# Kernel tuning notes

Measured on AMD Instinct MI355X. Metric: run time of the kernel, lower is better.

Reference implementation:

```python
import jax, jax.numpy as jnp
import numpy as np

N, E = 50000, 800000
IN_C, HID_C, OUT_C = 256, 256, 256


def setup_inputs() -> dict:
    key = jax.random.key(0)
    ks = jax.random.split(key, 8)
    x_piece = jax.random.normal(ks[0], (N, IN_C), dtype=jnp.float32)
    edge_index_piece = jax.random.randint(ks[1], (2, E), 0, N, dtype=jnp.int64)
    batch = jnp.zeros((N,), dtype=jnp.int64)
    def glorot(k, fan_in, fan_out):
        s = jnp.sqrt(6.0 / (fan_in + fan_out)).astype(jnp.float32)
        return jax.random.uniform(k, (fan_in, fan_out), jnp.float32, -s, s)
    return {
        "x_piece": x_piece,
        "edge_index_piece": edge_index_piece,
        "batch": batch,
        "W1": glorot(ks[2], IN_C, HID_C), "b1": jnp.zeros((HID_C,), jnp.float32),
        "W2": glorot(ks[3], HID_C, HID_C), "b2": jnp.zeros((HID_C,), jnp.float32),
        "W3": glorot(ks[4], HID_C, OUT_C), "b3": jnp.zeros((OUT_C,), jnp.float32),
    }


def _gcn_prep(edge_index, n_nodes):
    # add self-loops, compute symmetric normalization (PyG GCNConv default)
    src = jnp.concatenate([edge_index[0], jnp.arange(n_nodes, dtype=edge_index.dtype)])
    dst = jnp.concatenate([edge_index[1], jnp.arange(n_nodes, dtype=edge_index.dtype)])
    deg = jax.ops.segment_sum(jnp.ones_like(dst, dtype=jnp.float32), dst, num_segments=n_nodes)
    deg_inv_sqrt = jnp.where(deg > 0, jax.lax.rsqrt(jnp.maximum(deg, 1.0)), 0.0)
    norm = deg_inv_sqrt[src] * deg_inv_sqrt[dst]  # [E+N]
    return src, dst, norm


def _gcn_layer(x, src, dst, norm, W, b, n_nodes):
    h = x @ W                                   # [N, out] dense transform first
    msg = h[src] * norm[:, None]                # gather + scale
    out = jax.ops.segment_sum(msg, dst, num_segments=n_nodes)  # scatter-add
    return out + b


def reference(x_piece, edge_index_piece, batch, W1, b1, W2, b2, W3, b3):
    n_nodes = x_piece.shape[0]
    src, dst, norm = _gcn_prep(edge_index_piece, n_nodes)
    x = _gcn_layer(x_piece, src, dst, norm, W1, b1, n_nodes)
    x = jax.nn.gelu(x)
    x = _gcn_layer(x, src, dst, norm, W2, b2, n_nodes)
    x = jax.nn.gelu(x)
    x = _gcn_layer(x, src, dst, norm, W3, b3, n_nodes)
    return x
```

## Files before the change

### kernel.cpp

```cpp
#include <hip/hip_runtime.h>
#include <cstdint>
#include <cstddef>

#define CH 256

typedef _Float16 f16x8 __attribute__((ext_vector_type(8)));
typedef _Float16 f16x4 __attribute__((ext_vector_type(4)));
typedef float f32x4 __attribute__((ext_vector_type(4)));
typedef short short8 __attribute__((ext_vector_type(8)));

#define GLOB(x) ((const __attribute__((address_space(1))) void*)(x))
#define LDSP(x) ((__attribute__((address_space(3))) void*)(x))


__device__ __forceinline__ int ld_idx(const void* p, long long i, int w64) {
    if (w64) return (int)((const long long*)p)[i];
    return ((const int*)p)[i];
}

__device__ __forceinline__ float gelu_f(float x) {
    float x3 = x * x * x;
    float t = tanhf(0.7978845608028654f * (x + 0.044715f * x3));
    return 0.5f * x * (1.0f + t);
}


__global__ void k_detect(const void* __restrict__ ei, int* __restrict__ flag, int E) {
    int l = threadIdx.x;
    long long k = ((long long)l * (long long)(E - 1)) / 63;
    int w = ((const int*)ei)[2 * k + 1];
    unsigned long long vote = __ballot(w == 0);
    if (l == 0) *flag = (vote == ~0ULL) ? 1 : 0;
}

__global__ void k_deg(const void* __restrict__ ei, const int* __restrict__ flag,
                      int* __restrict__ deg, int E) {
    int e = blockIdx.x * blockDim.x + threadIdx.x;
    if (e >= E) return;
    int w64 = *flag;
    int d = ld_idx(ei, (long long)E + e, w64);
    atomicAdd(&deg[d], 1);
}

__global__ void k_scan_block(const int* __restrict__ deg, int* __restrict__ rowptr,
                             int* __restrict__ partial, int N) {
    __shared__ int s[256];
    int gid = blockIdx.x * 256 + threadIdx.x;
    int v = (gid < N) ? deg[gid] : 0;
    s[threadIdx.x] = v;
    __syncthreads();
    for (int off = 1; off < 256; off <<= 1) {
        int t = (threadIdx.x >= off) ? s[threadIdx.x - off] : 0;
        __syncthreads();
        s[threadIdx.x] += t;
        __syncthreads();
    }
    if (gid < N) rowptr[gid] = s[threadIdx.x] - v;
    if (threadIdx.x == 255) partial[blockIdx.x] = s[255];
}

__global__ void k_scan_partial(int* __restrict__ partial, int nb) {
    __shared__ int s[256];
    int i = threadIdx.x;
    int v = (i < nb) ? partial[i] : 0;
    s[i] = v;
    __syncthreads();
    for (int off = 1; off < 256; off <<= 1) {
        int t = (i >= off) ? s[i - off] : 0;
        __syncthreads();
        s[i] += t;
        __syncthreads();
    }
    if (i < nb) partial[i] = s[i] - v;
}

__global__ void k_add_off(int* __restrict__ rowptr, const int* __restrict__ partial,
                          const int* __restrict__ deg, float* __restrict__ dis,
                          int N, int E) {
    int gid = blockIdx.x * 256 + threadIdx.x;
    if (gid < N) {
        rowptr[gid] += partial[blockIdx.x];
        dis[gid] = 1.0f / sqrtf((float)(deg[gid] + 1));
    }
    if (gid == 0) rowptr[N] = E;
}

__global__ void k_scatter(const void* __restrict__ ei, const int* __restrict__ flag,
                          const int* __restrict__ rowptr, int* __restrict__ cnt,
                          int* __restrict__ ssrc, int E) {
    int e = blockIdx.x * blockDim.x + threadIdx.x;
    if (e >= E) return;
    int w64 = *flag;
    int s = ld_idx(ei, e, w64);
    int d = ld_idx(ei, (long long)E + e, w64);
    int pos = rowptr[d] + atomicAdd(&cnt[d], 1);
    ssrc[pos] = s;
}


__global__ void k_split_w3(const float* __restrict__ W1, const float* __restrict__ W2,
                           const float* __restrict__ W3, _Float16* __restrict__ Wh1,
                           _Float16* __restrict__ Wh2, _Float16* __restrict__ Wh3) {
    const float* W = (blockIdx.y == 0) ? W1 : (blockIdx.y == 1) ? W2 : W3;
    _Float16*   Wh = (blockIdx.y == 0) ? Wh1 : (blockIdx.y == 1) ? Wh2 : Wh3;
    int k = threadIdx.x;
    int c = blockIdx.x;
    Wh[c * CH + k] = (_Float16)W[k * CH + c];
}


__global__ __launch_bounds__(256) void k_quant_x(const float* __restrict__ x,
                                                 uint8_t* __restrict__ Xout,
                                                 float* __restrict__ sout, int N) {
    int node = blockIdx.x * 4 + threadIdx.y;
    if (node >= N) return;
    int lane = threadIdx.x;
    float4 v = ((const float4*)(x + (size_t)node * CH))[lane];
    float mx = fmaxf(fmaxf(fabsf(v.x), fabsf(v.y)), fmaxf(fabsf(v.z), fabsf(v.w)));
    #pragma unroll
    for (int off = 32; off > 0; off >>= 1)
        mx = fmaxf(mx, __shfl_xor(mx, off));
    float inv = (mx > 0.f) ? (32767.0f / mx) : 0.f;
    short4 q;
    q.x = (short)__float2int_rn(v.x * inv);
    q.y = (short)__float2int_rn(v.y * inv);
    q.z = (short)__float2int_rn(v.z * inv);
    q.w = (short)__float2int_rn(v.w * inv);
    *(short4*)(Xout + (size_t)node * 512 + (size_t)lane * 8) = q;
    if (lane == 0) sout[node] = mx * (1.0f / 32767.0f);
}


#define GM 128
#define GN 128
#define GK 32

__global__ __launch_bounds__(256, 2)
void k_gemm16(const uint8_t* __restrict__ X16, const float* __restrict__ sx,
              const _Float16* __restrict__ Bh, const float* __restrict__ dis,
              uint8_t* __restrict__ H16, float* __restrict__ hcomb, int M) {
    __shared__ __align__(16) char smem[65536];
    short*    lA16 = (short*)smem;
    _Float16* lB   = (_Float16*)(smem + 16384);

    const int tid  = threadIdx.x;
    const int lane = tid & 63;
    const int wid  = tid >> 6;
    const int m0   = blockIdx.x * GM;
    const int n0   = blockIdx.y * GN;
    const int wm   = wid >> 1, wn = wid & 1;
    const int r15  = lane & 15, kg = lane >> 4;

    auto stage = [&](int buf, int k0) {
        #pragma unroll
        for (int c = 0; c < 4; c++) {
            int call = wid * 4 + c;
            int cc = call & 7;
            int L = cc * 64 + lane;
            int row = L >> 2, ch = L & 3;
            int sch = ch ^ ((row >> 1) & 3);
            if (call < 8) {
                int gr = m0 + row; gr = (gr < M) ? gr : (M - 1);
                const uint8_t* g = X16 + (size_t)gr * 512 + (size_t)k0 * 2 + (sch << 4);
                __builtin_amdgcn_global_load_lds(GLOB(g), LDSP(&lA16[buf * 4096 + L * 8]), 16, 0, 0);
            } else {
                const _Float16* g = Bh + (size_t)(n0 + row) * CH + k0 + (sch << 3);
                __builtin_amdgcn_global_load_lds(GLOB(g), LDSP(&lB[buf * 4096 + L * 8]), 16, 0, 0);
            }
        }
    };

    f32x4 acc[4][4];
    #pragma unroll
    for (int i = 0; i < 4; i++)
        #pragma unroll
        for (int n = 0; n < 4; n++)
            acc[i][n] = (f32x4){0.f, 0.f, 0.f, 0.f};

    stage(0, 0);
    __syncthreads();

    for (int ks = 0; ks < 8; ks++) {
        int cur = ks & 1;
        if (ks < 7) stage(cur ^ 1, (ks + 1) * GK);

        f16x8 aq[4], bh[4];
        #pragma unroll
        for (int i = 0; i < 4; i++) {
            int R = wm * 64 + i * 16 + r15;
            int p = kg ^ ((R >> 1) & 3);
            short8 q = *(const short8*)&lA16[cur * 4096 + R * 32 + p * 8];
            #pragma unroll
            for (int j = 0; j < 8; j++)
                aq[i][j] = (_Float16)q[j];
        }
        #pragma unroll
        for (int n = 0; n < 4; n++) {
            int C = wn * 64 + n * 16 + r15;
            int p = kg ^ ((C >> 1) & 3);
            bh[n] = *(const f16x8*)&lB[cur * 4096 + C * GK + p * 8];
        }
        #pragma unroll
        for (int i = 0; i < 4; i++)
            #pragma unroll
            for (int n = 0; n < 4; n++)
                acc[i][n] = __builtin_amdgcn_mfma_f32_16x16x32_f16(aq[i], bh[n], acc[i][n], 0, 0, 0);
        __syncthreads();
    }

    float sC[4][4];
    #pragma unroll
    for (int i = 0; i < 4; i++)
        #pragma unroll
        for (int r = 0; r < 4; r++) {
            int gr = m0 + wm * 64 + i * 16 + kg * 4 + r;
            sC[i][r] = sx[(gr < M) ? gr : (M - 1)];
        }
    #pragma unroll
    for (int i = 0; i < 4; i++)
        #pragma unroll
        for (int n = 0; n < 4; n++)
            #pragma unroll
            for (int r = 0; r < 4; r++)
                acc[i][n][r] *= sC[i][r];

    float mx = 0.f;
    #pragma unroll
    for (int i = 0; i < 4; i++)
        #pragma unroll
        for (int n = 0; n < 4; n++)
            #pragma unroll
            for (int r = 0; r < 4; r++)
                mx = fmaxf(mx, fabsf(acc[i][n][r]));
    #pragma unroll
    for (int off = 32; off > 0; off >>= 1)
        mx = fmaxf(mx, __shfl_xor(mx, off));
    if (lane == 0) ((float*)smem)[wid] = mx;
    __syncthreads();
    float tmax = fmaxf(fmaxf(((float*)smem)[0], ((float*)smem)[1]),
                       fmaxf(((float*)smem)[2], ((float*)smem)[3]));
    float scl = tmax * (1.0f / 32767.0f);
    float inv = (tmax > 0.f) ? (32767.0f / tmax) : 0.f;
    __syncthreads();

    float* ep = (float*)smem + wid * 4096;
    #pragma unroll
    for (int i = 0; i < 4; i++)
        #pragma unroll
        for (int n = 0; n < 4; n++)
            #pragma unroll
            for (int r = 0; r < 4; r++)
                ep[(i * 16 + kg * 4 + r) * 64 + n * 16 + r15] = acc[i][n][r];
    __syncthreads();

    int q = lane & 15;
    int rsub = lane >> 4;
    #pragma unroll
    for (int p = 0; p < 16; p++) {
        int lrow = p * 4 + rsub;
        int grow = m0 + wm * 64 + lrow;
        if (grow < M) {
            int q0 = __float2int_rn(ep[lrow * 64 + q * 4 + 0] * inv);
            int q1 = __float2int_rn(ep[lrow * 64 + q * 4 + 1] * inv);
            int q2 = __float2int_rn(ep[lrow * 64 + q * 4 + 2] * inv);
            int q3 = __float2int_rn(ep[lrow * 64 + q * 4 + 3] * inv);
            uint2 d;
            d.x = (q0 & 0xFFFF) | (q1 << 16);
            d.y = (q2 & 0xFFFF) | (q3 << 16);
            int col = n0 + wn * 64 + q * 4;
            *(uint2*)(H16 + (size_t)grow * 512 + (size_t)col * 2) = d;
        }
    }

    if (tid < GM && m0 + tid < M)
        hcomb[(size_t)(m0 + tid) * 2 + (n0 >> 7)] = scl * dis[m0 + tid];
}


template <int MODE>
__global__ __launch_bounds__(256) void k_agg(const uint8_t* __restrict__ H16,
                                             const float* __restrict__ hcomb,
                                             const float* __restrict__ dis,
                                             const int* __restrict__ rowptr,
                                             const int* __restrict__ ssrc,
                                             const float* __restrict__ bias,
                                             float* __restrict__ out,
                                             uint8_t* __restrict__ Xout,
                                             float* __restrict__ sxout, int N) {
    int node = blockIdx.x * 4 + threadIdx.y;
    if (node >= N) return;
    int lane = threadIdx.x;
    int half = lane >> 5;
    float d = dis[node];
    short4 hv = *(const short4*)(H16 + (size_t)node * 512 + (size_t)lane * 8);
    float wself = d * hcomb[(size_t)node * 2 + half];
    float ax = wself * (float)hv.x, ay = wself * (float)hv.y;
    float az = wself * (float)hv.z, aw = wself * (float)hv.w;
    int s = rowptr[node], e = rowptr[node + 1];
    int j = s;
    for (; j + 8 <= e; j += 8) {
        int p[8];
        #pragma unroll
        for (int t = 0; t < 8; t++) p[t] = ssrc[j + t];
        short4 v[8];
        float sc[8];
        #pragma unroll
        for (int t = 0; t < 8; t++) {
            v[t] = *(const short4*)(H16 + (size_t)p[t] * 512 + (size_t)lane * 8);
            sc[t] = hcomb[(size_t)p[t] * 2 + half];
        }
        #pragma unroll
        for (int t = 0; t < 8; t++) {
            float wn = d * sc[t];
            ax += wn * (float)v[t].x; ay += wn * (float)v[t].y;
            az += wn * (float)v[t].z; aw += wn * (float)v[t].w;
        }
    }
    for (; j < e; j++) {
        int p = ssrc[j];
        float wn = d * hcomb[(size_t)p * 2 + half];
        short4 v = *(const short4*)(H16 + (size_t)p * 512 + (size_t)lane * 8);
        ax += wn * (float)v.x; ay += wn * (float)v.y;
        az += wn * (float)v.z; aw += wn * (float)v.w;
    }
    float4 b = ((const float4*)bias)[lane];
    ax += b.x; ay += b.y; az += b.z; aw += b.w;
    if (MODE == 0) {
        ax = gelu_f(ax); ay = gelu_f(ay); az = gelu_f(az); aw = gelu_f(aw);
        float mx = fmaxf(fmaxf(fabsf(ax), fabsf(ay)), fmaxf(fabsf(az), fabsf(aw)));
        #pragma unroll
        for (int off = 32; off > 0; off >>= 1)
            mx = fmaxf(mx, __shfl_xor(mx, off));
        float inv = (mx > 0.f) ? (32767.0f / mx) : 0.f;
        short4 q;
        q.x = (short)__float2int_rn(ax * inv);
        q.y = (short)__float2int_rn(ay * inv);
        q.z = (short)__float2int_rn(az * inv);
        q.w = (short)__float2int_rn(aw * inv);
        *(short4*)(Xout + (size_t)node * 512 + (size_t)lane * 8) = q;
        if (lane == 0) sxout[node] = mx * (1.0f / 32767.0f);
    } else {
        ((float4*)(out + (size_t)node * CH))[lane] = make_float4(ax, ay, az, aw);
    }
}


extern "C" void kernel_launch(void* const* d_in, const int* in_sizes, int n_in,
                              void* d_out, int out_size, void* d_ws, size_t ws_size,
                              hipStream_t stream) {
    const float* x  = (const float*)d_in[0];
    const void*  ei = d_in[1];
    const float* W1 = (const float*)d_in[3]; const float* b1 = (const float*)d_in[4];
    const float* W2 = (const float*)d_in[5]; const float* b2 = (const float*)d_in[6];
    const float* W3 = (const float*)d_in[7]; const float* b3 = (const float*)d_in[8];

    int N = in_sizes[0] / CH;
    int E = in_sizes[1] / 2;
    float* out = (float*)d_out;

    char* ws = (char*)d_ws;
    auto take = [&](size_t bytes) {
        char* p = ws;
        ws += (bytes + 15) & ~(size_t)15;
        return p;
    };
    uint8_t*  H16    = (uint8_t*) take((size_t)N * 512);
    uint8_t*  Xa     = (uint8_t*) take((size_t)N * 512);
    uint8_t*  Xb     = (uint8_t*) take((size_t)N * 512);
    float*    hcomb  = (float*)   take((size_t)N * 2 * sizeof(float));
    float*    sxa    = (float*)   take((size_t)N * sizeof(float));
    float*    sxb    = (float*)   take((size_t)N * sizeof(float));
    int*      deg    = (int*)     take((size_t)N * sizeof(int));
    float*    dis    = (float*)   take((size_t)N * sizeof(float));
    int*      rowptr = (int*)     take((size_t)(N + 1) * sizeof(int));
    int*      cnt    = (int*)     take((size_t)N * sizeof(int));
    int*      part   = (int*)     take(4096);
    int*      flag   = (int*)     take(16);
    int*      ssrc   = (int*)     take((size_t)E * sizeof(int));
    _Float16* Wh1    = (_Float16*)take((size_t)CH * CH * 2);
    _Float16* Wh2    = (_Float16*)take((size_t)CH * CH * 2);
    _Float16* Wh3    = (_Float16*)take((size_t)CH * CH * 2);

    hipMemsetAsync(deg, 0, (size_t)N * sizeof(int), stream);
    hipMemsetAsync(cnt, 0, (size_t)N * sizeof(int), stream);

    int eb = (E + 255) / 256;
    int nb = (N + 255) / 256;

    k_detect<<<1, 64, 0, stream>>>(ei, flag, E);
    k_deg<<<eb, 256, 0, stream>>>(ei, flag, deg, E);
    k_scan_block<<<nb, 256, 0, stream>>>(deg, rowptr, part, N);
    k_scan_partial<<<1, 256, 0, stream>>>(part, nb);
    k_add_off<<<nb, 256, 0, stream>>>(rowptr, part, deg, dis, N, E);
    k_scatter<<<eb, 256, 0, stream>>>(ei, flag, rowptr, cnt, ssrc, E);

    dim3 wgrid(CH, 3);
    k_split_w3<<<wgrid, CH, 0, stream>>>(W1, W2, W3, Wh1, Wh2, Wh3);

    dim3 qgrid((N + 3) / 4);
    dim3 qblock(64, 4);
    k_quant_x<<<qgrid, qblock, 0, stream>>>(x, Xa, sxa, N);

    dim3 ggrid((N + GM - 1) / GM, CH / GN);
    dim3 agrid((N + 3) / 4);
    dim3 ablock(64, 4);

    k_gemm16<<<ggrid, 256, 0, stream>>>(Xa, sxa, Wh1, dis, H16, hcomb, N);
    k_agg<0><<<agrid, ablock, 0, stream>>>(H16, hcomb, dis, rowptr, ssrc, b1, out, Xb, sxb, N);
    k_gemm16<<<ggrid, 256, 0, stream>>>(Xb, sxb, Wh2, dis, H16, hcomb, N);
    k_agg<0><<<agrid, ablock, 0, stream>>>(H16, hcomb, dis, rowptr, ssrc, b2, out, Xa, sxa, N);
    k_gemm16<<<ggrid, 256, 0, stream>>>(Xa, sxa, Wh3, dis, H16, hcomb, N);
    k_agg<1><<<agrid, ablock, 0, stream>>>(H16, hcomb, dis, rowptr, ssrc, b3, out, Xb, sxb, N);
}
```

Before: 385.6 us.

## Fuse graph preprocessing, weight conversion and input quantization into one cooperative kernel

Replaces eight separate launches and two memsets (detect, degree count, block scan, partial scan, offset add, CSR scatter, weight transpose and x quantization) with a single cooperative kernel that uses grid-wide syncs between phases. Independent work such as weight conversion and x quantization now shares the first phase with zeroing. This removes launch gaps and tail effects of the small kernels. In exchange it adds grid.sync barriers, and it relies on a fixed 1024-block grid being co-resident. That grid size may leave the memory-bound phases with less parallelism than the original full-size grids had.

```diff
diff --git a/kernel.cpp b/kernel.cpp
--- a/kernel.cpp
+++ b/kernel.cpp
@@ -1,8 +1,11 @@
 #include <hip/hip_runtime.h>
+#include <hip/hip_cooperative_groups.h>
 #include <cstdint>
 #include <cstddef>
 
 #define CH 256
+
+namespace cg = cooperative_groups;
 
 typedef _Float16 f16x8 __attribute__((ext_vector_type(8)));
 typedef _Float16 f16x4 __attribute__((ext_vector_type(4)));
@@ -25,109 +28,108 @@
 }
 
 
-__global__ void k_detect(const void* __restrict__ ei, int* __restrict__ flag, int E) {
-    int l = threadIdx.x;
-    long long k = ((long long)l * (long long)(E - 1)) / 63;
-    int w = ((const int*)ei)[2 * k + 1];
-    unsigned long long vote = __ballot(w == 0);
-    if (l == 0) *flag = (vote == ~0ULL) ? 1 : 0;
-}
-
-__global__ void k_deg(const void* __restrict__ ei, const int* __restrict__ flag,
-                      int* __restrict__ deg, int E) {
-    int e = blockIdx.x * blockDim.x + threadIdx.x;
-    if (e >= E) return;
+__global__ __launch_bounds__(256)
+void k_prep(const void* __restrict__ ei, const float* __restrict__ x,
+            const float* __restrict__ W1, const float* __restrict__ W2,
+            const float* __restrict__ W3,
+            int* __restrict__ flag, int* __restrict__ deg, int* __restrict__ cnt,
+            int* __restrict__ rowptr, int* __restrict__ partial, float* __restrict__ dis,
+            int* __restrict__ ssrc, uint8_t* __restrict__ Xa, float* __restrict__ sxa,
+            _Float16* __restrict__ Wh1, _Float16* __restrict__ Wh2,
+            _Float16* __restrict__ Wh3, int N, int E) {
+    cg::grid_group grid = cg::this_grid();
+    const int tid   = threadIdx.x;
+    const int gsize = gridDim.x * 256;
+    const int gid0  = blockIdx.x * 256 + tid;
+    __shared__ int s[256];
+
+    if (blockIdx.x == 0 && tid < 64) {
+        long long k = ((long long)tid * (long long)(E - 1)) / 63;
+        int w = ((const int*)ei)[2 * k + 1];
+        unsigned long long vote = __ballot(w == 0);
+        if (tid == 0) *flag = (vote == ~0ULL) ? 1 : 0;
+    }
+    for (int i = gid0; i < N; i += gsize) { deg[i] = 0; cnt[i] = 0; }
+    for (int i = gid0; i < 3 * CH * CH; i += gsize) {
+        int l = i >> 16;
+        int r = i & 65535;
+        const float* W = (l == 0) ? W1 : (l == 1) ? W2 : W3;
+        _Float16*   Wh = (l == 0) ? Wh1 : (l == 1) ? Wh2 : Wh3;
+        Wh[r] = (_Float16)W[(r & 255) * CH + (r >> 8)];
+    }
+    {
+        int wave = gid0 >> 6, lane = tid & 63;
+        int nwaves = gsize >> 6;
+        for (int node = wave; node < N; node += nwaves) {
+            float4 v = ((const float4*)(x + (size_t)node * CH))[lane];
+            float mx = fmaxf(fmaxf(fabsf(v.x), fabsf(v.y)), fmaxf(fabsf(v.z), fabsf(v.w)));
+            #pragma unroll
+            for (int off = 32; off > 0; off >>= 1)
+                mx = fmaxf(mx, __shfl_xor(mx, off));
+            float inv = (mx > 0.f) ? (32767.0f / mx) : 0.f;
+            short4 q;
+            q.x = (short)__float2int_rn(v.x * inv);
+            q.y = (short)__float2int_rn(v.y * inv);
+            q.z = (short)__float2int_rn(v.z * inv);
+            q.w = (short)__float2int_rn(v.w * inv);
+            *(short4*)(Xa + (size_t)node * 512 + (size_t)lane * 8) = q;
+            if (lane == 0) sxa[node] = mx * (1.0f / 32767.0f);
+        }
+    }
+    grid.sync();
+
     int w64 = *flag;
-    int d = ld_idx(ei, (long long)E + e, w64);
-    atomicAdd(&deg[d], 1);
-}
-
-__global__ void k_scan_block(const int* __restrict__ deg, int* __restrict__ rowptr,
-                             int* __restrict__ partial, int N) {
-    __shared__ int s[256];
-    int gid = blockIdx.x * 256 + threadIdx.x;
-    int v = (gid < N) ? deg[gid] : 0;
-    s[threadIdx.x] = v;
-    __syncthreads();
-    for (int off = 1; off < 256; off <<= 1) {
-        int t = (threadIdx.x >= off) ? s[threadIdx.x - off] : 0;
+    for (int e = gid0; e < E; e += gsize) {
+        int d = ld_idx(ei, (long long)E + e, w64);
+        atomicAdd(&deg[d], 1);
+    }
+    grid.sync();
+
+    int nb = (N + 255) / 256;
+    for (int b = blockIdx.x; b < nb; b += gridDim.x) {
+        int g = b * 256 + tid;
+        int v = (g < N) ? deg[g] : 0;
+        s[tid] = v;
         __syncthreads();
-        s[threadIdx.x] += t;
+        for (int off = 1; off < 256; off <<= 1) {
+            int t = (tid >= off) ? s[tid - off] : 0;
+            __syncthreads();
+            s[tid] += t;
+            __syncthreads();
+        }
+        if (g < N) rowptr[g] = s[tid] - v;
+        if (tid == 255) partial[b] = s[255];
         __syncthreads();
     }
-    if (gid < N) rowptr[gid] = s[threadIdx.x] - v;
-    if (threadIdx.x == 255) partial[blockIdx.x] = s[255];
-}
-
-__global__ void k_scan_partial(int* __restrict__ partial, int nb) {
-    __shared__ int s[256];
-    int i = threadIdx.x;
-    int v = (i < nb) ? partial[i] : 0;
-    s[i] = v;
-    __syncthreads();
-    for (int off = 1; off < 256; off <<= 1) {
-        int t = (i >= off) ? s[i - off] : 0;
+    grid.sync();
+
+    if (blockIdx.x == 0) {
+        int v = (tid < nb) ? partial[tid] : 0;
+        s[tid] = v;
         __syncthreads();
-        s[i] += t;
-        __syncthreads();
-    }
-    if (i < nb) partial[i] = s[i] - v;
-}
-
-__global__ void k_add_off(int* __restrict__ rowptr, const int* __restrict__ partial,
-                          const int* __restrict__ deg, float* __restrict__ dis,
-                          int N, int E) {
-    int gid = blockIdx.x * 256 + threadIdx.x;
-    if (gid < N) {
-        rowptr[gid] += partial[blockIdx.x];
-        dis[gid] = 1.0f / sqrtf((float)(deg[gid] + 1));
-    }
-    if (gid == 0) rowptr[N] = E;
-}
-
-__global__ void k_scatter(const void* __restrict__ ei, const int* __restrict__ flag,
-                          const int* __restrict__ rowptr, int* __restrict__ cnt,
-                          int* __restrict__ ssrc, int E) {
-    int e = blockIdx.x * blockDim.x + threadIdx.x;
-    if (e >= E) return;
-    int w64 = *flag;
-    int s = ld_idx(ei, e, w64);
-    int d = ld_idx(ei, (long long)E + e, w64);
-    int pos = rowptr[d] + atomicAdd(&cnt[d], 1);
-    ssrc[pos] = s;
-}
-
-
-__global__ void k_split_w3(const float* __restrict__ W1, const float* __restrict__ W2,
-                           const float* __restrict__ W3, _Float16* __restrict__ Wh1,
-                           _Float16* __restrict__ Wh2, _Float16* __restrict__ Wh3) {
-    const float* W = (blockIdx.y == 0) ? W1 : (blockIdx.y == 1) ? W2 : W3;
-    _Float16*   Wh = (blockIdx.y == 0) ? Wh1 : (blockIdx.y == 1) ? Wh2 : Wh3;
-    int k = threadIdx.x;
-    int c = blockIdx.x;
-    Wh[c * CH + k] = (_Float16)W[k * CH + c];
-}
-
-
-__global__ __launch_bounds__(256) void k_quant_x(const float* __restrict__ x,
-                                                 uint8_t* __restrict__ Xout,
-                                                 float* __restrict__ sout, int N) {
-    int node = blockIdx.x * 4 + threadIdx.y;
-    if (node >= N) return;
-    int lane = threadIdx.x;
-    float4 v = ((const float4*)(x + (size_t)node * CH))[lane];
-    float mx = fmaxf(fmaxf(fabsf(v.x), fabsf(v.y)), fmaxf(fabsf(v.z), fabsf(v.w)));
-    #pragma unroll
-    for (int off = 32; off > 0; off >>= 1)
-        mx = fmaxf(mx, __shfl_xor(mx, off));
-    float inv = (mx > 0.f) ? (32767.0f / mx) : 0.f;
-    short4 q;
-    q.x = (short)__float2int_rn(v.x * inv);
-    q.y = (short)__float2int_rn(v.y * inv);
-    q.z = (short)__float2int_rn(v.z * inv);
-    q.w = (short)__float2int_rn(v.w * inv);
-    *(short4*)(Xout + (size_t)node * 512 + (size_t)lane * 8) = q;
-    if (lane == 0) sout[node] = mx * (1.0f / 32767.0f);
+        for (int off = 1; off < 256; off <<= 1) {
+            int t = (tid >= off) ? s[tid - off] : 0;
+            __syncthreads();
+            s[tid] += t;
+            __syncthreads();
+        }
+        if (tid < nb) partial[tid] = s[tid] - v;
+    }
+    grid.sync();
+
+    for (int i = gid0; i < N; i += gsize) {
+        rowptr[i] += partial[i >> 8];
+        dis[i] = 1.0f / sqrtf((float)(deg[i] + 1));
+    }
+    if (gid0 == 0) rowptr[N] = E;
+    grid.sync();
+
+    for (int e = gid0; e < E; e += gsize) {
+        int sidx = ld_idx(ei, e, w64);
+        int d = ld_idx(ei, (long long)E + e, w64);
+        int pos = rowptr[d] + atomicAdd(&cnt[d], 1);
+        ssrc[pos] = sidx;
+    }
 }
 
 
@@ -348,8 +350,8 @@
 extern "C" void kernel_launch(void* const* d_in, const int* in_sizes, int n_in,
                               void* d_out, int out_size, void* d_ws, size_t ws_size,
                               hipStream_t stream) {
+    const void*  ei = d_in[1];
     const float* x  = (const float*)d_in[0];
-    const void*  ei = d_in[1];
     const float* W1 = (const float*)d_in[3]; const float* b1 = (const float*)d_in[4];
     const float* W2 = (const float*)d_in[5]; const float* b2 = (const float*)d_in[6];
     const float* W3 = (const float*)d_in[7]; const float* b3 = (const float*)d_in[8];
@@ -381,25 +383,14 @@
     _Float16* Wh2    = (_Float16*)take((size_t)CH * CH * 2);
     _Float16* Wh3    = (_Float16*)take((size_t)CH * CH * 2);
 
-    hipMemsetAsync(deg, 0, (size_t)N * sizeof(int), stream);
-    hipMemsetAsync(cnt, 0, (size_t)N * sizeof(int), stream);
-
-    int eb = (E + 255) / 256;
-    int nb = (N + 255) / 256;
-
-    k_detect<<<1, 64, 0, stream>>>(ei, flag, E);
-    k_deg<<<eb, 256, 0, stream>>>(ei, flag, deg, E);
-    k_scan_block<<<nb, 256, 0, stream>>>(deg, rowptr, part, N);
-    k_scan_partial<<<1, 256, 0, stream>>>(part, nb);
-    k_add_off<<<nb, 256, 0, stream>>>(rowptr, part, deg, dis, N, E);
-    k_scatter<<<eb, 256, 0, stream>>>(ei, flag, rowptr, cnt, ssrc, E);
-
-    dim3 wgrid(CH, 3);
-    k_split_w3<<<wgrid, CH, 0, stream>>>(W1, W2, W3, Wh1, Wh2, Wh3);
-
-    dim3 qgrid((N + 3) / 4);
-    dim3 qblock(64, 4);
-    k_quant_x<<<qgrid, qblock, 0, stream>>>(x, Xa, sxa, N);
+    {
+        void* pargs[] = {(void*)&ei, (void*)&x, (void*)&W1, (void*)&W2, (void*)&W3,
+                         (void*)&flag, (void*)&deg, (void*)&cnt, (void*)&rowptr,
+                         (void*)&part, (void*)&dis, (void*)&ssrc, (void*)&Xa,
+                         (void*)&sxa, (void*)&Wh1, (void*)&Wh2, (void*)&Wh3,
+                         (void*)&N, (void*)&E};
+        hipLaunchCooperativeKernel((void*)k_prep, dim3(1024), dim3(256), pargs, 0, stream);
+    }
 
     dim3 ggrid((N + GM - 1) / GM, CH / GN);
     dim3 agrid((N + 3) / 4);
```

Result: slower. 906.4 us (+135.1%).
